# Kernel tuning notes

Measured on AMD Instinct MI355X. Metric: run time of the kernel, lower is better.

The kernel has to match this reference:

```python
import jax, jax.numpy as jnp
import numpy as np

HOP_LENGTH = 160
SAMPLE_RATE = 16000
CHUNK_LENGTH = 30
N_SAMPLES = SAMPLE_RATE * CHUNK_LENGTH          # 480000
N_FRAMES = N_SAMPLES // HOP_LENGTH              # 3000
N_FFT = 400
N_FREQ = 1 + N_FFT // 2                         # 201
N_MELS = 80
REFLECT_PAD = N_FFT // 2                        # 200
BATCH = 64


def _make_reflect_indices():
    left = np.arange(REFLECT_PAD, 0, -1, dtype=np.int32)
    center = np.arange(N_SAMPLES, dtype=np.int32)
    right = np.arange(N_SAMPLES - 2, N_SAMPLES - REFLECT_PAD - 2, -1, dtype=np.int32)
    return np.concatenate([left, center, right], axis=0)  # [480400]


def _make_stft_conv_kernels():
    n = np.arange(N_FFT, dtype=np.float32)
    k = np.arange(N_FREQ, dtype=np.float32)[:, None]
    window = (0.5 - 0.5 * np.cos(2.0 * np.pi * n / float(N_FFT)))[None, :]  # periodic Hann
    phase = 2.0 * np.pi / float(N_FFT) * (k * n[None, :])
    real = (np.cos(phase) * window).astype(np.float32)[:, None, :]   # [201,1,400]
    imag = (-np.sin(phase) * window).astype(np.float32)[:, None, :]  # [201,1,400]
    return real, imag


_REFLECT_IDX = jnp.asarray(_make_reflect_indices())
_REAL_K, _IMAG_K = (jnp.asarray(a) for a in _make_stft_conv_kernels())
_INV_LN10 = np.float32(1.0 / np.log(10.0))


def setup_inputs() -> dict:
    key = jax.random.key(0)
    k1, k2, k3 = jax.random.split(key, 3)
    waveform = jax.random.normal(k1, (BATCH, N_SAMPLES), dtype=jnp.float32)
    valid_samples = jax.random.randint(k2, (BATCH,), 0, N_SAMPLES).astype(jnp.int32)
    mel_filters = jax.random.uniform(k3, (N_FREQ, N_MELS), dtype=jnp.float32)
    return {"waveform": waveform, "valid_samples": valid_samples, "mel_filters": mel_filters}


def reference(waveform, valid_samples, mel_filters):
    # Reflect-pad via gather: [B, 480400]
    x = waveform[:, _REFLECT_IDX][:, None, :]  # [B,1,480400]
    dn = ('NCH', 'OIH', 'NCH')
    real = jax.lax.conv_general_dilated(x, _REAL_K, (HOP_LENGTH,), 'VALID', dimension_numbers=dn)
    imag = jax.lax.conv_general_dilated(x, _IMAG_K, (HOP_LENGTH,), 'VALID', dimension_numbers=dn)
    power = (real * real + imag * imag)[:, :, :N_FRAMES]          # [B,201,3000]
    mel = jnp.einsum('bft,fm->bmt', power, mel_filters)            # [B,80,3000]
    log_spec = jnp.log(jnp.maximum(mel, 1e-10)) * _INV_LN10
    max_val = jnp.max(log_spec, axis=(1, 2), keepdims=True)
    log_spec = jnp.maximum(log_spec, max_val - 8.0)
    input_features = (log_spec + 4.0) / 4.0
    frame_starts = jnp.arange(0, N_SAMPLES, HOP_LENGTH, dtype=jnp.int32)[None, :]  # [1,3000]
    feature_attention_mask = (frame_starts < valid_samples[:, None]).astype(jnp.int32)
    return input_features, feature_attention_mask
```

## Files before the change

kernel.cpp:

```cpp
#include <hip/hip_runtime.h>
#include <hip/hip_bf16.h>

#define NSAMP   480000
#define NFRAMES 3000
#define NFFT    400
#define NFREQ   201
#define NMELS   80
#define HOP     160
#define BATCH   64
#define TT      64
#define TBLK    47
#define NPAIR   7
#define KF      13
#define MKSTEPS 7
#define PWS     232
#define PROW    208
#define OBS     68
#define SREG    (2 * KF * 512)
#define DOFF    SREG
#define LDS_USH (2 * SREG)
#define SCHUNKS (2 * KF * 64)
#define FEAT_ELEMS (BATCH * NMELS * NFRAMES)
#define OUT_ELEMS  (FEAT_ELEMS + BATCH * NFRAMES)
#define NF4     (FEAT_ELEMS / 4)
#define NM4     ((BATCH * NFRAMES) / 4)
#define TWO_PI  6.283185307179586f
#define WC_ELEMS (NPAIR * KF * 64 * 8)
#define MFRAG_ELEMS (5 * MKSTEPS * 64 * 8)
#define WC_BYTES (WC_ELEMS * 2)
#define MFRAG_BYTES (MFRAG_ELEMS * 2)
#define WMAX_OFF  (2 * WC_BYTES + MFRAG_BYTES)
#define POWER_OFF (WMAX_OFF + 256)
#define POWER_BYTES ((size_t)BATCH * NFRAMES * PROW * 2)

typedef __attribute__((ext_vector_type(8))) short bf16x8;
typedef __attribute__((ext_vector_type(8))) ushort ushort8;
typedef __attribute__((ext_vector_type(4))) float f32x4;
typedef __attribute__((ext_vector_type(16))) float f32x16;

static __device__ __forceinline__ ushort f2bf(float x) {
    __hip_bfloat16 h = __float2bfloat16(x);
    return *reinterpret_cast<ushort*>(&h);
}
static __device__ __forceinline__ ushort tbf(float x) {
    return (ushort)(__float_as_uint(x) >> 16);
}
static __device__ __forceinline__ int refl(int idx) {
    idx = (idx < 0) ? -idx : idx;
    return (idx >= NSAMP) ? (2 * NSAMP - 2 - idx) : idx;
}

__global__ __launch_bounds__(256)
void fill_tables_k(ushort* __restrict__ wc, ushort* __restrict__ wsn,
                   ushort* __restrict__ mfr, const float* __restrict__ mf,
                   unsigned* __restrict__ wmax) {
    const int t = blockIdx.x * 256 + threadIdx.x;
    if (t < WC_ELEMS / 8) {
        const int lane = t & 63;
        const int fk = t >> 6;
        const int ks = fk % KF;
        const int nf = fk / KF;
        const int f = nf * 32 + (lane & 31);
        const int kbase = ks * 16 + 8 * (lane >> 5);
        #pragma unroll
        for (int j = 0; j < 8; ++j) {
            const int km = kbase + j;
            float vc = 0.f, vs = 0.f;
            if (f <= 200 && km >= 1 && km <= 200) {
                const float win = 0.5f - 0.5f * cosf(TWO_PI * (float)km / (float)NFFT);
                const int r = (f * km) % NFFT;
                const float ph = (float)r * (TWO_PI / (float)NFFT);
                float sv, cv;
                sincosf(ph, &sv, &cv);
                vc = win * cv;
                vs = -win * sv;
                if (km == 200) vc *= 0.5f;
            }
            wc [(size_t)t * 8 + j] = f2bf(vc);
            wsn[(size_t)t * 8 + j] = f2bf(vs);
        }
    } else if (t < WC_ELEMS / 8 + MFRAG_ELEMS / 8) {
        const int u = t - WC_ELEMS / 8;
        const int lane = u & 63;
        const int fk = u >> 6;
        const int ks = fk % MKSTEPS;
        const int Mf = fk / MKSTEPS;
        const int mel = Mf * 16 + (lane & 15);
        const int kbase = ks * 32 + 8 * (lane >> 4);
        #pragma unroll
        for (int j = 0; j < 8; ++j) {
            const int freq = kbase + j;
            const float val = (freq < NFREQ) ? mf[freq * NMELS + mel] : 0.f;
            mfr[(size_t)u * 8 + j] = f2bf(val);
        }
    }
    if (blockIdx.x == 0 && threadIdx.x < BATCH) wmax[threadIdx.x] = 0u;
}

__global__ __launch_bounds__(512, 4)
void stft_power_k(const float* __restrict__ wav, const ushort* __restrict__ wcos,
                  const ushort* __restrict__ wsin, ushort* __restrict__ pwg) {
    __shared__ __align__(16) ushort lds[LDS_USH];

    const int b   = blockIdx.y;
    const int t0  = blockIdx.x * TT;
    const int tid = threadIdx.x;
    const int l   = tid & 63;
    const int wv  = tid >> 6;
    const float* w = wav + (size_t)b * NSAMP;
    const int g0 = t0 * HOP - (NFFT / 2);

    for (int c = tid; c < SCHUNKS; c += 512) {
        const int cl = c & 63;
        const int fk = c >> 6;
        const int ks = fk % KF;
        const int m  = fk / KF;
        const int r  = m * 32 + (cl & 31);
        const int kb = ks * 16 + 8 * (cl >> 5);
        const int fs = g0 + r * HOP;
        ushort8 us, ud;
        if (fs >= 0 && fs + 401 <= NSAMP) {
            const float4 f0 = *reinterpret_cast<const float4*>(w + fs + kb);
            const float4 f1 = *reinterpret_cast<const float4*>(w + fs + kb + 4);
            const int ba = fs + 392 - kb;
            const float4 q0 = *reinterpret_cast<const float4*>(w + ba);
            const float4 q1 = *reinterpret_cast<const float4*>(w + ba + 4);
            const float4 q2 = *reinterpret_cast<const float4*>(w + ba + 8);
            const float F[8] = {f0.x, f0.y, f0.z, f0.w, f1.x, f1.y, f1.z, f1.w};
            const float R[8] = {q2.x, q1.w, q1.z, q1.y, q1.x, q0.w, q0.z, q0.y};
            #pragma unroll
            for (int j = 0; j < 8; ++j) {
                us[j] = tbf(F[j] + R[j]);
                ud[j] = tbf(F[j] - R[j]);
            }
        } else {
            #pragma unroll
            for (int j = 0; j < 8; ++j) {
                const float a = w[refl(fs + kb + j)];
                const float c2 = w[refl(fs + 400 - kb - j)];
                us[j] = f2bf(a + c2);
                ud[j] = f2bf(a - c2);
            }
        }
        const int base = ((m * KF + ks) << 9) + (cl << 3);
        *reinterpret_cast<ushort8*>(&lds[base]) = us;
        *reinterpret_cast<ushort8*>(&lds[DOFF + base]) = ud;
    }
    __syncthreads();

    f32x16 accC[2], accS[2];
    #pragma unroll
    for (int m = 0; m < 2; ++m)
        #pragma unroll
        for (int j = 0; j < 16; ++j) { accC[m][j] = 0.f; accS[m][j] = 0.f; }

    if (wv < NPAIR) {
        const ushort* gC = wcos + ((size_t)(wv * KF) << 9) + (l << 3);
        const ushort* gS = wsin + ((size_t)(wv * KF) << 9) + (l << 3);
        const int aOff = l << 3;

        bf16x8 As[2][2], Ad[2][2], Bc[2], Bs[2];
        #pragma unroll
        for (int m = 0; m < 2; ++m) {
            As[0][m] = *reinterpret_cast<const bf16x8*>(lds + ((m * KF) << 9) + aOff);
            Ad[0][m] = *reinterpret_cast<const bf16x8*>(lds + DOFF + ((m * KF) << 9) + aOff);
        }
        Bc[0] = *reinterpret_cast<const bf16x8*>(gC);
        Bs[0] = *reinterpret_cast<const bf16x8*>(gS);

        #pragma unroll
        for (int ks = 0; ks < KF; ++ks) {
            const int cur = ks & 1, nxt = cur ^ 1;
            if (ks + 1 < KF) {
                #pragma unroll
                for (int m = 0; m < 2; ++m) {
                    As[nxt][m] = *reinterpret_cast<const bf16x8*>(
                        lds + ((m * KF + ks + 1) << 9) + aOff);
                    Ad[nxt][m] = *reinterpret_cast<const bf16x8*>(
                        lds + DOFF + ((m * KF + ks + 1) << 9) + aOff);
                }
                Bc[nxt] = *reinterpret_cast<const bf16x8*>(gC + ((size_t)(ks + 1) << 9));
                Bs[nxt] = *reinterpret_cast<const bf16x8*>(gS + ((size_t)(ks + 1) << 9));
            }
            accC[0] = __builtin_amdgcn_mfma_f32_32x32x16_bf16(As[cur][0], Bc[cur], accC[0], 0, 0, 0);
            accC[1] = __builtin_amdgcn_mfma_f32_32x32x16_bf16(As[cur][1], Bc[cur], accC[1], 0, 0, 0);
            accS[0] = __builtin_amdgcn_mfma_f32_32x32x16_bf16(Ad[cur][0], Bs[cur], accS[0], 0, 0, 0);
            accS[1] = __builtin_amdgcn_mfma_f32_32x32x16_bf16(Ad[cur][1], Bs[cur], accS[1], 0, 0, 0);
        }
    }
    __syncthreads();

    for (int i = tid; i < TT * 7; i += 512) {
        const int r = i / 7;
        const int cc = 201 + i - r * 7;
        lds[r * PWS + cc] = 0;
    }
    if (wv < NPAIR) {
        const int f = wv * 32 + (l & 31);
        #pragma unroll
        for (int m = 0; m < 2; ++m) {
            #pragma unroll
            for (int reg = 0; reg < 16; ++reg) {
                const float p = accC[m][reg] * accC[m][reg] + accS[m][reg] * accS[m][reg];
                const int fr = m * 32 + (reg & 3) + 8 * (reg >> 2) + 4 * (l >> 5);
                if (f < NFREQ) lds[fr * PWS + f] = f2bf(p);
            }
        }
    }
    __syncthreads();

    for (int c = tid; c < TT * 26; c += 512) {
        const int row = c / 26;
        const int c8  = (c - row * 26) * 8;
        const int rg  = t0 + row;
        if (rg < NFRAMES) {
            const ushort8 v = *reinterpret_cast<const ushort8*>(&lds[row * PWS + c8]);
            *reinterpret_cast<ushort8*>(&pwg[((size_t)b * NFRAMES + rg) * PROW + c8]) = v;
        }
    }
}

__global__ __launch_bounds__(256, 5)
void mel_k(const ushort* __restrict__ pwg, const ushort* __restrict__ mfrag,
           float* __restrict__ out, unsigned* __restrict__ wmax) {
    __shared__ __align__(16) ushort pw[TT * PWS];
    float* outb = reinterpret_cast<float*>(pw);

    const int b   = blockIdx.y;
    const int t0  = blockIdx.x * TT;
    const int tid = threadIdx.x;
    const int l   = tid & 63;
    const int wv  = tid >> 6;

    for (int c = tid; c < TT * 26; c += 256) {
        const int row = c / 26;
        const int c8  = (c - row * 26) * 8;
        const int rg  = t0 + row;
        ushort8 v = (ushort8)(0);
        if (rg < NFRAMES)
            v = *reinterpret_cast<const ushort8*>(&pwg[((size_t)b * NFRAMES + rg) * PROW + c8]);
        *reinterpret_cast<ushort8*>(&pw[row * PWS + c8]) = v;
    }
    for (int i = tid; i < TT * 24; i += 256) {
        const int row = i / 24;
        const int cc = 208 + i - row * 24;
        pw[row * PWS + cc] = 0;
    }
    __syncthreads();

    float res[5][4];
    #pragma unroll
    for (int q = 0; q < 5; ++q) {
        const int tile = wv + 4 * q;
        const int Mf = tile >> 2;
        const int ff = tile & 3;
        f32x4 mc = (f32x4){0.f, 0.f, 0.f, 0.f};
        #pragma unroll
        for (int ks = 0; ks < MKSTEPS; ++ks) {
            const bf16x8 aT = *reinterpret_cast<const bf16x8*>(
                mfrag + ((size_t)(Mf * MKSTEPS + ks) * 64 + l) * 8);
            const bf16x8 bP = *reinterpret_cast<const bf16x8*>(
                pw + (ff * 16 + (l & 15)) * PWS + 8 * (l >> 4) + 32 * ks);
            mc = __builtin_amdgcn_mfma_f32_16x16x32_bf16(aT, bP, mc, 0, 0, 0);
        }
        #pragma unroll
        for (int r = 0; r < 4; ++r) res[q][r] = mc[r];
    }
    __syncthreads();

    float lmax = -3.0e38f;
    #pragma unroll
    for (int q = 0; q < 5; ++q) {
        const int tile = wv + 4 * q;
        const int Mf = tile >> 2;
        const int ff = tile & 3;
        #pragma unroll
        for (int r = 0; r < 4; ++r) {
            const float v = log10f(fmaxf(res[q][r], 1e-10f));
            const int mel = Mf * 16 + 4 * (l >> 4) + r;
            const int frame = ff * 16 + (l & 15);
            outb[mel * OBS + frame] = v;
            if (t0 + frame < NFRAMES) lmax = fmaxf(lmax, v);
        }
    }
    __syncthreads();

    for (int c2 = tid; c2 < NMELS * 16; c2 += 256) {
        const int mel = c2 >> 4;
        const int f4  = (c2 & 15) * 4;
        if (t0 + f4 < NFRAMES) {
            float4 v;
            v.x = outb[mel * OBS + f4];
            v.y = outb[mel * OBS + f4 + 1];
            v.z = outb[mel * OBS + f4 + 2];
            v.w = outb[mel * OBS + f4 + 3];
            *reinterpret_cast<float4*>(
                &out[((size_t)b * NMELS + mel) * NFRAMES + t0 + f4]) = v;
        }
    }

    #pragma unroll
    for (int off = 32; off > 0; off >>= 1)
        lmax = fmaxf(lmax, __shfl_xor(lmax, off));
    if (l == 0) {
        const unsigned bits = __float_as_uint(lmax);
        const unsigned key = bits ^ ((bits & 0x80000000u) ? 0xFFFFFFFFu : 0x80000000u);
        atomicMax(&wmax[b], key);
    }
}

__global__ __launch_bounds__(256)
void finalize_k(float* __restrict__ out, const unsigned* __restrict__ wmax,
                const int* __restrict__ valid) {
    const int i4 = blockIdx.x * 256 + threadIdx.x;
    if (i4 < NF4) {
        const int b = i4 / (NMELS * NFRAMES / 4);
        const unsigned key = wmax[b];
        const unsigned bits = key ^ ((key & 0x80000000u) ? 0x80000000u : 0xFFFFFFFFu);
        const float mx8 = __uint_as_float(bits) - 8.0f;
        float4 v = *reinterpret_cast<float4*>(&out[(size_t)i4 * 4]);
        v.x = (fmaxf(v.x, mx8) + 4.0f) * 0.25f;
        v.y = (fmaxf(v.y, mx8) + 4.0f) * 0.25f;
        v.z = (fmaxf(v.z, mx8) + 4.0f) * 0.25f;
        v.w = (fmaxf(v.w, mx8) + 4.0f) * 0.25f;
        *reinterpret_cast<float4*>(&out[(size_t)i4 * 4]) = v;
    } else if (i4 < NF4 + NM4) {
        const int j4 = i4 - NF4;
        const int bb = j4 / (NFRAMES / 4);
        const int tf0 = (j4 - bb * (NFRAMES / 4)) * 4;
        const int vs = valid[bb];
        float4 m;
        m.x = ((tf0 + 0) * HOP < vs) ? 1.0f : 0.0f;
        m.y = ((tf0 + 1) * HOP < vs) ? 1.0f : 0.0f;
        m.z = ((tf0 + 2) * HOP < vs) ? 1.0f : 0.0f;
        m.w = ((tf0 + 3) * HOP < vs) ? 1.0f : 0.0f;
        *reinterpret_cast<float4*>(&out[FEAT_ELEMS + (size_t)j4 * 4]) = m;
    }
}

extern "C" void kernel_launch(void* const* d_in, const int* in_sizes, int n_in,
                              void* d_out, int out_size, void* d_ws, size_t ws_size,
                              hipStream_t stream) {
    const float* wav   = (const float*)d_in[0];
    const int*   valid = (const int*)d_in[1];
    const float* mf    = (const float*)d_in[2];
    float* out = (float*)d_out;

    ushort*   wcos  = (ushort*)d_ws;
    ushort*   wsin  = (ushort*)((char*)d_ws + WC_BYTES);
    ushort*   mfrag = (ushort*)((char*)d_ws + 2 * WC_BYTES);
    unsigned* wmax  = (unsigned*)((char*)d_ws + WMAX_OFF);
    ushort*   pwg   = (ushort*)((char*)d_ws + POWER_OFF);

    const int fill_items = WC_ELEMS / 8 + MFRAG_ELEMS / 8;
    fill_tables_k<<<(fill_items + 255) / 256, 256, 0, stream>>>(wcos, wsin, mfrag, mf, wmax);
    dim3 g(TBLK, BATCH);
    stft_power_k<<<g, 512, 0, stream>>>(wav, wcos, wsin, pwg);
    mel_k<<<g, 256, 0, stream>>>(pwg, mfrag, out, wmax);
    finalize_k<<<(NF4 + NM4 + 255) / 256, 256, 0, stream>>>(out, wmax, valid);
}
```

Measured before the change: 213.3 us.

## Make mel kernel persistent over four time tiles with register prefetch

Each mel_k block now loops over up to four consecutive 64-frame tiles instead of one, so the grid shrinks from 47 to 12 blocks per batch item. The next tile's power data is prefetched into registers while the current tile runs its MFMA and log10 work, and the per-block atomicMax is issued once instead of four times. The cost is fewer blocks in flight (768 versus about 3000), an extra barrier per tile, and higher register pressure from the prefetch buffers.

Result: slower. 248.6 us (+16.5%).

```diff
diff --git a/kernel.cpp b/kernel.cpp
--- a/kernel.cpp
+++ b/kernel.cpp
@@ -10,6 +10,7 @@
 #define BATCH   64
 #define TT      64
 #define TBLK    47
+#define MTBLK   12
 #define NPAIR   7
 #define KF      13
 #define MKSTEPS 7
@@ -226,77 +227,105 @@
     __shared__ __align__(16) ushort pw[TT * PWS];
     float* outb = reinterpret_cast<float*>(pw);
 
-    const int b   = blockIdx.y;
-    const int t0  = blockIdx.x * TT;
-    const int tid = threadIdx.x;
-    const int l   = tid & 63;
-    const int wv  = tid >> 6;
-
-    for (int c = tid; c < TT * 26; c += 256) {
-        const int row = c / 26;
-        const int c8  = (c - row * 26) * 8;
-        const int rg  = t0 + row;
-        ushort8 v = (ushort8)(0);
-        if (rg < NFRAMES)
-            v = *reinterpret_cast<const ushort8*>(&pwg[((size_t)b * NFRAMES + rg) * PROW + c8]);
-        *reinterpret_cast<ushort8*>(&pw[row * PWS + c8]) = v;
-    }
-    for (int i = tid; i < TT * 24; i += 256) {
-        const int row = i / 24;
-        const int cc = 208 + i - row * 24;
-        pw[row * PWS + cc] = 0;
-    }
-    __syncthreads();
-
-    float res[5][4];
-    #pragma unroll
-    for (int q = 0; q < 5; ++q) {
-        const int tile = wv + 4 * q;
-        const int Mf = tile >> 2;
-        const int ff = tile & 3;
-        f32x4 mc = (f32x4){0.f, 0.f, 0.f, 0.f};
-        #pragma unroll
-        for (int ks = 0; ks < MKSTEPS; ++ks) {
-            const bf16x8 aT = *reinterpret_cast<const bf16x8*>(
-                mfrag + ((size_t)(Mf * MKSTEPS + ks) * 64 + l) * 8);
-            const bf16x8 bP = *reinterpret_cast<const bf16x8*>(
-                pw + (ff * 16 + (l & 15)) * PWS + 8 * (l >> 4) + 32 * ks);
-            mc = __builtin_amdgcn_mfma_f32_16x16x32_bf16(aT, bP, mc, 0, 0, 0);
-        }
-        #pragma unroll
-        for (int r = 0; r < 4; ++r) res[q][r] = mc[r];
-    }
-    __syncthreads();
+    const int b    = blockIdx.y;
+    const int st0  = blockIdx.x * 4;
+    const int nst  = (st0 + 4 <= TBLK) ? 4 : (TBLK - st0);
+    const int tid  = threadIdx.x;
+    const int l    = tid & 63;
+    const int wv   = tid >> 6;
+
+    ushort8 pre[7];
+    #define LOAD_TILE(T0)                                                        \
+        _Pragma("unroll")                                                        \
+        for (int j = 0; j < 7; ++j) {                                            \
+            const int c = tid + j * 256;                                         \
+            ushort8 v = (ushort8)(0);                                            \
+            if (c < TT * 26) {                                                   \
+                const int row = c / 26;                                          \
+                const int c8  = (c - row * 26) * 8;                              \
+                const int rg  = (T0) + row;                                      \
+                if (rg < NFRAMES)                                                \
+                    v = *reinterpret_cast<const ushort8*>(                       \
+                        &pwg[((size_t)b * NFRAMES + rg) * PROW + c8]);           \
+            }                                                                    \
+            pre[j] = v;                                                          \
+        }
+
+    LOAD_TILE(st0 * TT);
 
     float lmax = -3.0e38f;
-    #pragma unroll
-    for (int q = 0; q < 5; ++q) {
-        const int tile = wv + 4 * q;
-        const int Mf = tile >> 2;
-        const int ff = tile & 3;
-        #pragma unroll
-        for (int r = 0; r < 4; ++r) {
-            const float v = log10f(fmaxf(res[q][r], 1e-10f));
-            const int mel = Mf * 16 + 4 * (l >> 4) + r;
-            const int frame = ff * 16 + (l & 15);
-            outb[mel * OBS + frame] = v;
-            if (t0 + frame < NFRAMES) lmax = fmaxf(lmax, v);
-        }
-    }
-    __syncthreads();
-
-    for (int c2 = tid; c2 < NMELS * 16; c2 += 256) {
-        const int mel = c2 >> 4;
-        const int f4  = (c2 & 15) * 4;
-        if (t0 + f4 < NFRAMES) {
-            float4 v;
-            v.x = outb[mel * OBS + f4];
-            v.y = outb[mel * OBS + f4 + 1];
-            v.z = outb[mel * OBS + f4 + 2];
-            v.w = outb[mel * OBS + f4 + 3];
-            *reinterpret_cast<float4*>(
-                &out[((size_t)b * NMELS + mel) * NFRAMES + t0 + f4]) = v;
-        }
+
+    for (int st = 0; st < nst; ++st) {
+        const int t0 = (st0 + st) * TT;
+
+        #pragma unroll
+        for (int j = 0; j < 7; ++j) {
+            const int c = tid + j * 256;
+            if (c < TT * 26) {
+                const int row = c / 26;
+                const int c8  = (c - row * 26) * 8;
+                *reinterpret_cast<ushort8*>(&pw[row * PWS + c8]) = pre[j];
+            }
+        }
+        for (int i = tid; i < TT * 24; i += 256) {
+            const int row = i / 24;
+            const int cc = 208 + i - row * 24;
+            pw[row * PWS + cc] = 0;
+        }
+        __syncthreads();
+
+        if (st + 1 < nst) LOAD_TILE((st0 + st + 1) * TT);
+
+        float res[5][4];
+        #pragma unroll
+        for (int q = 0; q < 5; ++q) {
+            const int tile = wv + 4 * q;
+            const int Mf = tile >> 2;
+            const int ff = tile & 3;
+            f32x4 mc = (f32x4){0.f, 0.f, 0.f, 0.f};
+            #pragma unroll
+            for (int ks = 0; ks < MKSTEPS; ++ks) {
+                const bf16x8 aT = *reinterpret_cast<const bf16x8*>(
+                    mfrag + ((size_t)(Mf * MKSTEPS + ks) * 64 + l) * 8);
+                const bf16x8 bP = *reinterpret_cast<const bf16x8*>(
+                    pw + (ff * 16 + (l & 15)) * PWS + 8 * (l >> 4) + 32 * ks);
+                mc = __builtin_amdgcn_mfma_f32_16x16x32_bf16(aT, bP, mc, 0, 0, 0);
+            }
+            #pragma unroll
+            for (int r = 0; r < 4; ++r) res[q][r] = mc[r];
+        }
+        __syncthreads();
+
+        #pragma unroll
+        for (int q = 0; q < 5; ++q) {
+            const int tile = wv + 4 * q;
+            const int Mf = tile >> 2;
+            const int ff = tile & 3;
+            #pragma unroll
+            for (int r = 0; r < 4; ++r) {
+                const float v = log10f(fmaxf(res[q][r], 1e-10f));
+                const int mel = Mf * 16 + 4 * (l >> 4) + r;
+                const int frame = ff * 16 + (l & 15);
+                outb[mel * OBS + frame] = v;
+                if (t0 + frame < NFRAMES) lmax = fmaxf(lmax, v);
+            }
+        }
+        __syncthreads();
+
+        for (int c2 = tid; c2 < NMELS * 16; c2 += 256) {
+            const int mel = c2 >> 4;
+            const int f4  = (c2 & 15) * 4;
+            if (t0 + f4 < NFRAMES) {
+                float4 v;
+                v.x = outb[mel * OBS + f4];
+                v.y = outb[mel * OBS + f4 + 1];
+                v.z = outb[mel * OBS + f4 + 2];
+                v.w = outb[mel * OBS + f4 + 3];
+                *reinterpret_cast<float4*>(
+                    &out[((size_t)b * NMELS + mel) * NFRAMES + t0 + f4]) = v;
+            }
+        }
+        __syncthreads();
     }
 
     #pragma unroll
@@ -307,6 +336,7 @@
         const unsigned key = bits ^ ((bits & 0x80000000u) ? 0xFFFFFFFFu : 0x80000000u);
         atomicMax(&wmax[b], key);
     }
+    #undef LOAD_TILE
 }
 
 __global__ __launch_bounds__(256)
@@ -354,8 +384,7 @@
 
     const int fill_items = WC_ELEMS / 8 + MFRAG_ELEMS / 8;
     fill_tables_k<<<(fill_items + 255) / 256, 256, 0, stream>>>(wcos, wsin, mfrag, mf, wmax);
-    dim3 g(TBLK, BATCH);
-    stft_power_k<<<g, 512, 0, stream>>>(wav, wcos, wsin, pwg);
-    mel_k<<<g, 256, 0, stream>>>(pwg, mfrag, out, wmax);
+    stft_power_k<<<dim3(TBLK, BATCH), 512, 0, stream>>>(wav, wcos, wsin, pwg);
+    mel_k<<<dim3(MTBLK, BATCH), 256, 0, stream>>>(pwg, mfrag, out, wmax);
     finalize_k<<<(NF4 + NM4 + 255) / 256, 256, 0, stream>>>(out, wmax, valid);
 }
```
